# Optimization experiments

Hardware: AMD Instinct MI355X
Metric: run time of the kernel (lower is better)

The kernel has to match this reference:

```python
import jax, jax.numpy as jnp
import numpy as np

N_CLASSES = 5
N_SAMPLES = 512
D_EMB = 512


def setup_inputs() -> dict:
    key = jax.random.key(0)
    k1, k2, k3 = jax.random.split(key, 3)
    prediction = jax.random.normal(k1, (N_SAMPLES, D_EMB), dtype=jnp.float32)
    target = jax.random.randint(k2, (N_SAMPLES,), 0, N_CLASSES)
    # learnable_map=None -> all learnable, init = inverse_softplus(0.5 + 0.5*U[0,1))
    t = 0.5 + 0.5 * jax.random.uniform(k3, (N_CLASSES - 1,), dtype=jnp.float32)
    distances_raw = jnp.log(jnp.exp(t) - 1.0)  # inverse softplus (t < 20 always)
    return {"prediction": prediction, "distances_raw": distances_raw, "target": target}


def reference(prediction, distances_raw, target):
    n = prediction.shape[0]
    eps = 1e-8  # torch F.cosine_similarity eps
    xn = prediction / jnp.maximum(jnp.linalg.norm(prediction, axis=1, keepdims=True), eps)
    cos = xn @ xn.T  # [i, j] pairwise cosine similarity

    same = target[:, None] == target[None, :]          # label_diff <= 0
    positives = same & ~jnp.eye(n, dtype=bool)          # same label, not self
    negatives = ~same                                   # different label

    # ordinal class positions from softplus-parameterized gaps
    pos_d = jax.nn.softplus(distances_raw)
    class_pos = jnp.concatenate([jnp.zeros(1, dtype=pos_d.dtype), jnp.cumsum(pos_d)])
    cp = class_pos[target]
    margins = jnp.where(negatives, jnp.abs(cp[:, None] - cp[None, :]), 0.0)  # [i, j]

    # Original loop over anchor-positive columns k:
    #   n_pair_loss[k][i, j] = -cos[i, k] + cos[i, j] + margins[i, j]
    #   valid iff positives[i, k] and negatives[i, j]; invalid -> relu(-inf)=0
    base = cos + margins                                # [i, j]
    diff = base[:, None, :] - cos[:, :, None]           # [i, k, j]
    val = jnp.where(negatives[:, None, :], jax.nn.relu(diff), 0.0)
    s = jnp.where(positives, val.sum(axis=2), 0.0)      # [i, k]
    negcount = negatives.sum(axis=1)                    # [i]
    cnt = jnp.where(positives, negcount[:, None], 0)    # loss_mask2
    L = s / jnp.maximum(cnt, 1)                         # per (anchor i, positive k)

    # mean over nonzero entries (mean_n_pair_loss[mean_n_pair_loss != 0].mean())
    nz = (L != 0.0).sum()
    return L.sum() / jnp.maximum(nz, 1).astype(L.dtype)
```

## Files before the change

### kernel.cpp

```cpp
#include <hip/hip_runtime.h>
#include <math.h>

#define NS 512
#define DE 512
#define NCL 5
#define NBLK 256


__global__ __launch_bounds__(512, 2) void k_dots(const float* __restrict__ pred,
                                                 float* __restrict__ dotA,
                                                 float* __restrict__ dotB,
                                                 float* __restrict__ dg) {
    const int b = blockIdx.x;
    const int tid = threadIdx.x;
    const int iA = b, iB = b + 256;

    const int w = tid >> 6, lane = tid & 63;
    const int g = lane >> 4, s = lane & 15;

    const float4* pA = (const float4*)&pred[(size_t)iA * DE];
    const float4* pB = (const float4*)&pred[(size_t)iB * DE];
    float4 fA[8], fB[8];
#pragma unroll
    for (int p = 0; p < 8; p++) { fA[p] = pA[p * 16 + s]; fB[p] = pB[p * 16 + s]; }

#pragma unroll 4
    for (int t = 0; t < 16; t++) {
        const int j = w * 64 + t * 4 + g;
        const float4* rj = (const float4*)&pred[(size_t)j * DE];
        float4 x[8];
#pragma unroll
        for (int p = 0; p < 8; p++) x[p] = rj[p * 16 + s];
        float aA = 0.0f, aB = 0.0f, aS = 0.0f;
#pragma unroll
        for (int p = 0; p < 8; p++) {
            aA = fmaf(x[p].x, fA[p].x, aA); aA = fmaf(x[p].y, fA[p].y, aA);
            aA = fmaf(x[p].z, fA[p].z, aA); aA = fmaf(x[p].w, fA[p].w, aA);
            aB = fmaf(x[p].x, fB[p].x, aB); aB = fmaf(x[p].y, fB[p].y, aB);
            aB = fmaf(x[p].z, fB[p].z, aB); aB = fmaf(x[p].w, fB[p].w, aB);
            aS = fmaf(x[p].x, x[p].x, aS);  aS = fmaf(x[p].y, x[p].y, aS);
            aS = fmaf(x[p].z, x[p].z, aS);  aS = fmaf(x[p].w, x[p].w, aS);
        }
#pragma unroll
        for (int m = 1; m <= 8; m <<= 1) {
            aA += __shfl_xor(aA, m);
            aB += __shfl_xor(aB, m);
            aS += __shfl_xor(aS, m);
        }
        if (s == 0) {
            dotA[(size_t)b * NS + j] = aA;
            dotB[(size_t)b * NS + j] = aB;
            if (b == 0) dg[j] = aS;
        }
    }
}

__global__ __launch_bounds__(512) void k_loss(const float* __restrict__ dotA,
                                              const float* __restrict__ dotB,
                                              const float* __restrict__ dg,
                                              const int* __restrict__ target,
                                              const float* __restrict__ draw,
                                              unsigned int* __restrict__ ctrl,
                                              float* __restrict__ out) {
    const int b = blockIdx.x;
    const int tid = threadIdx.x;
    const int iA = b, iB = b + 256;

    __shared__ float  rn_s[NS];
    __shared__ float  ckA[NS], ckB[NS];
    __shared__ float4 v4sA[NS / 4], v4sB[NS / 4];
    __shared__ int    pkA[NS], pkB[NS];
    __shared__ float  spart[NS * 17];
    __shared__ float  redf[512];
    __shared__ int    redi[512];
    __shared__ unsigned int pcA, pcB;

    float* gsum = (float*)ctrl;
    unsigned int* gnz    = ctrl + 1;
    unsigned int* ticket = ctrl + 2;

    if (tid == 0) { pcA = 0u; pcB = 0u; }

    const int j = tid;
    const float da = dotA[(size_t)b * NS + j];
    const float db = dotB[(size_t)b * NS + j];
    const float ns = dg[j];
    const float rnj = 1.0f / fmaxf(sqrtf(ns), 1e-8f);
    rn_s[j] = rnj;

    float cp[NCL];
    cp[0] = 0.0f;
#pragma unroll
    for (int c = 0; c < NCL - 1; c++) cp[c + 1] = cp[c] + log1pf(expf(draw[c]));
    const int tiA = target[iA], tiB = target[iB];
    const float cpA = cp[tiA], cpB = cp[tiB];
    const int tj = target[j];
    const float cpj = cp[tj];
    __syncthreads();

    const float rniA = rn_s[iA], rniB = rn_s[iB];
    {
        float c0 = da * rniA * rnj;
        bool n0 = (tj != tiA);
        ckA[j] = c0;
        ((float*)v4sA)[j] = n0 ? (c0 + fabsf(cpA - cpj)) : -1e30f;
        if (!n0 && j != iA) pkA[atomicAdd(&pcA, 1u)] = j;
        redi[tid] = (n0 ? 1 : 0);
    }
    {
        float c0 = db * rniB * rnj;
        bool n0 = (tj != tiB);
        ckB[j] = c0;
        ((float*)v4sB)[j] = n0 ? (c0 + fabsf(cpB - cpj)) : -1e30f;
        if (!n0 && j != iB) pkB[atomicAdd(&pcB, 1u)] = j;
        redi[tid] += (n0 ? 1 : 0) << 16;
    }
    __syncthreads();
    for (int s2 = 256; s2 > 0; s2 >>= 1) {
        if (tid < s2) redi[tid] += redi[tid + s2];
        __syncthreads();
    }
    const int negA = redi[0] & 0xffff;
    const int negB = redi[0] >> 16;
    const unsigned int nposA = pcA, nposB = pcB;
    __syncthreads();

    const int kl = tid & 31, jc = tid >> 5;
    const float denA = (float)(negA > 1 ? negA : 1);
    const float denB = (float)(negB > 1 ? negB : 1);
    float contrib = 0.0f;
    int nzc = 0;

    {
        float4 vj[8];
#pragma unroll
        for (int t = 0; t < 8; t++) vj[t] = v4sA[jc * 8 + t];
        for (unsigned int p = kl; p < nposA; p += 32) {
            const float ckp = ckA[pkA[p]];
            float s0 = 0.0f, s1 = 0.0f;
#pragma unroll
            for (int t = 0; t < 8; t++) {
                float4 wv = vj[t];
                s0 += fmaxf(wv.x - ckp, 0.0f) + fmaxf(wv.y - ckp, 0.0f);
                s1 += fmaxf(wv.z - ckp, 0.0f) + fmaxf(wv.w - ckp, 0.0f);
            }
            spart[p * 17 + jc] = s0 + s1;
        }
        __syncthreads();
        for (unsigned int p = tid; p < nposA; p += 512) {
            float s0 = 0.0f;
#pragma unroll
            for (int q = 0; q < 16; q++) s0 += spart[p * 17 + q];
            contrib += s0 / denA;
            if (s0 != 0.0f) nzc++;
        }
        __syncthreads();
    }
    {
        float4 vj[8];
#pragma unroll
        for (int t = 0; t < 8; t++) vj[t] = v4sB[jc * 8 + t];
        for (unsigned int p = kl; p < nposB; p += 32) {
            const float ckp = ckB[pkB[p]];
            float s0 = 0.0f, s1 = 0.0f;
#pragma unroll
            for (int t = 0; t < 8; t++) {
                float4 wv = vj[t];
                s0 += fmaxf(wv.x - ckp, 0.0f) + fmaxf(wv.y - ckp, 0.0f);
                s1 += fmaxf(wv.z - ckp, 0.0f) + fmaxf(wv.w - ckp, 0.0f);
            }
            spart[p * 17 + jc] = s0 + s1;
        }
        __syncthreads();
        for (unsigned int p = tid; p < nposB; p += 512) {
            float s0 = 0.0f;
#pragma unroll
            for (int q = 0; q < 16; q++) s0 += spart[p * 17 + q];
            contrib += s0 / denB;
            if (s0 != 0.0f) nzc++;
        }
    }

    redf[tid] = contrib;
    redi[tid] = nzc;
    __syncthreads();
    for (int s2 = 256; s2 > 0; s2 >>= 1) {
        if (tid < s2) { redf[tid] += redf[tid + s2]; redi[tid] += redi[tid + s2]; }
        __syncthreads();
    }
    if (tid == 0) {
        if (redf[0] != 0.0f || redi[0] != 0) {
            atomicAdd(gsum, redf[0]);
            atomicAdd(gnz, (unsigned int)redi[0]);
        }
        __threadfence();
        unsigned int t = atomicAdd(ticket, 1u);
        if (t == (unsigned int)(NBLK - 1)) {
            float s0 = atomicAdd(gsum, 0.0f);
            unsigned int n = atomicAdd(gnz, 0u);
            out[0] = s0 / (float)(n > 1u ? n : 1u);
        }
    }
}

extern "C" void kernel_launch(void* const* d_in, const int* in_sizes, int n_in,
                              void* d_out, int out_size, void* d_ws, size_t ws_size,
                              hipStream_t stream) {
    const float* pred   = (const float*)d_in[0];
    const float* draw   = (const float*)d_in[1];
    const int*   target = (const int*)d_in[2];
    float* out = (float*)d_out;

    float* ws   = (float*)d_ws;
    float* dotA = ws;
    float* dotB = ws + NBLK * NS;
    float* dg   = ws + 2 * NBLK * NS;
    unsigned int* ctrl = (unsigned int*)(dg + NS);

    hipMemsetAsync(ctrl, 0, 4 * sizeof(unsigned int), stream);
    hipLaunchKernelGGL(k_dots, dim3(NBLK), dim3(512), 0, stream, pred, dotA, dotB, dg);
    hipLaunchKernelGGL(k_loss, dim3(NBLK), dim3(512), 0, stream,
                       dotA, dotB, dg, target, draw, ctrl, out);
}
```

Measured before the change: 87.73 us.

## Retile Gram kernel into 16x64 output tiles over a 2D grid

The dot-product kernel now computes a 16-row by 64-column block of the Gram matrix per workgroup on a 32x8 grid. Each thread holds two j-rows and 16 anchor rows in registers, so every loaded vector is reused across many outputs instead of recomputing two anchors against all 512 rows. Results are staged through shared memory for coalesced stores into a single dots matrix. This cuts redundant global loads, but the per-thread register footprint is much larger and there are many more cross-lane shuffle reductions.

```diff
diff --git a/kernel.cpp b/kernel.cpp
--- a/kernel.cpp
+++ b/kernel.cpp
@@ -8,55 +8,70 @@
 
 
 __global__ __launch_bounds__(512, 2) void k_dots(const float* __restrict__ pred,
-                                                 float* __restrict__ dotA,
-                                                 float* __restrict__ dotB,
+                                                 float* __restrict__ dots,
                                                  float* __restrict__ dg) {
-    const int b = blockIdx.x;
+    const int a0 = blockIdx.x * 16;
+    const int j0 = blockIdx.y * 64;
     const int tid = threadIdx.x;
-    const int iA = b, iB = b + 256;
-
     const int w = tid >> 6, lane = tid & 63;
     const int g = lane >> 4, s = lane & 15;
-
-    const float4* pA = (const float4*)&pred[(size_t)iA * DE];
-    const float4* pB = (const float4*)&pred[(size_t)iB * DE];
-    float4 fA[8], fB[8];
-#pragma unroll
-    for (int p = 0; p < 8; p++) { fA[p] = pA[p * 16 + s]; fB[p] = pB[p * 16 + s]; }
-
-#pragma unroll 4
-    for (int t = 0; t < 16; t++) {
-        const int j = w * 64 + t * 4 + g;
-        const float4* rj = (const float4*)&pred[(size_t)j * DE];
-        float4 x[8];
-#pragma unroll
-        for (int p = 0; p < 8; p++) x[p] = rj[p * 16 + s];
-        float aA = 0.0f, aB = 0.0f, aS = 0.0f;
-#pragma unroll
-        for (int p = 0; p < 8; p++) {
-            aA = fmaf(x[p].x, fA[p].x, aA); aA = fmaf(x[p].y, fA[p].y, aA);
-            aA = fmaf(x[p].z, fA[p].z, aA); aA = fmaf(x[p].w, fA[p].w, aA);
-            aB = fmaf(x[p].x, fB[p].x, aB); aB = fmaf(x[p].y, fB[p].y, aB);
-            aB = fmaf(x[p].z, fB[p].z, aB); aB = fmaf(x[p].w, fB[p].w, aB);
-            aS = fmaf(x[p].x, x[p].x, aS);  aS = fmaf(x[p].y, x[p].y, aS);
-            aS = fmaf(x[p].z, x[p].z, aS);  aS = fmaf(x[p].w, x[p].w, aS);
-        }
-#pragma unroll
-        for (int m = 1; m <= 8; m <<= 1) {
-            aA += __shfl_xor(aA, m);
-            aB += __shfl_xor(aB, m);
-            aS += __shfl_xor(aS, m);
-        }
-        if (s == 0) {
-            dotA[(size_t)b * NS + j] = aA;
-            dotB[(size_t)b * NS + j] = aB;
-            if (b == 0) dg[j] = aS;
-        }
-    }
+    const int jl0 = (w * 4 + g) * 2;
+
+    __shared__ float tile[16][65];
+    __shared__ float stile[64];
+
+    const float4* p4 = (const float4*)pred;
+    const float4* pj0 = p4 + (size_t)(j0 + jl0) * (DE / 4);
+    const float4* pj1 = p4 + (size_t)(j0 + jl0 + 1) * (DE / 4);
+
+    float acc0[17] = {};
+    float acc1[17] = {};
+
+#pragma unroll 2
+    for (int kb = 0; kb < 8; kb++) {
+        float4 fa[16];
+#pragma unroll
+        for (int a = 0; a < 16; a++)
+            fa[a] = p4[(size_t)(a0 + a) * (DE / 4) + kb * 16 + s];
+        float4 x0 = pj0[kb * 16 + s];
+        float4 x1 = pj1[kb * 16 + s];
+#pragma unroll
+        for (int a = 0; a < 16; a++) {
+            acc0[a] = fmaf(x0.x, fa[a].x, acc0[a]); acc0[a] = fmaf(x0.y, fa[a].y, acc0[a]);
+            acc0[a] = fmaf(x0.z, fa[a].z, acc0[a]); acc0[a] = fmaf(x0.w, fa[a].w, acc0[a]);
+            acc1[a] = fmaf(x1.x, fa[a].x, acc1[a]); acc1[a] = fmaf(x1.y, fa[a].y, acc1[a]);
+            acc1[a] = fmaf(x1.z, fa[a].z, acc1[a]); acc1[a] = fmaf(x1.w, fa[a].w, acc1[a]);
+        }
+        acc0[16] = fmaf(x0.x, x0.x, acc0[16]); acc0[16] = fmaf(x0.y, x0.y, acc0[16]);
+        acc0[16] = fmaf(x0.z, x0.z, acc0[16]); acc0[16] = fmaf(x0.w, x0.w, acc0[16]);
+        acc1[16] = fmaf(x1.x, x1.x, acc1[16]); acc1[16] = fmaf(x1.y, x1.y, acc1[16]);
+        acc1[16] = fmaf(x1.z, x1.z, acc1[16]); acc1[16] = fmaf(x1.w, x1.w, acc1[16]);
+    }
+
+#pragma unroll
+    for (int m = 1; m <= 8; m <<= 1) {
+#pragma unroll
+        for (int a = 0; a < 17; a++) {
+            acc0[a] += __shfl_xor(acc0[a], m);
+            acc1[a] += __shfl_xor(acc1[a], m);
+        }
+    }
+
+    tile[s][jl0]     = acc0[s];
+    tile[s][jl0 + 1] = acc1[s];
+    if (s == 0) { stile[jl0] = acc0[16]; stile[jl0 + 1] = acc1[16]; }
+    __syncthreads();
+
+#pragma unroll
+    for (int r = 0; r < 2; r++) {
+        int idx = tid + r * 512;
+        int a = idx >> 6, jl = idx & 63;
+        dots[(size_t)(a0 + a) * NS + j0 + jl] = tile[a][jl];
+    }
+    if (tid < 64) dg[j0 + tid] = stile[tid];
 }
 
-__global__ __launch_bounds__(512) void k_loss(const float* __restrict__ dotA,
-                                              const float* __restrict__ dotB,
+__global__ __launch_bounds__(512) void k_loss(const float* __restrict__ dots,
                                               const float* __restrict__ dg,
                                               const int* __restrict__ target,
                                               const float* __restrict__ draw,
@@ -82,8 +97,8 @@
     if (tid == 0) { pcA = 0u; pcB = 0u; }
 
     const int j = tid;
-    const float da = dotA[(size_t)b * NS + j];
-    const float db = dotB[(size_t)b * NS + j];
+    const float da = dots[(size_t)iA * NS + j];
+    const float db = dots[(size_t)iB * NS + j];
     const float ns = dg[j];
     const float rnj = 1.0f / fmaxf(sqrtf(ns), 1e-8f);
     rn_s[j] = rnj;
@@ -212,13 +227,12 @@
     float* out = (float*)d_out;
 
     float* ws   = (float*)d_ws;
-    float* dotA = ws;
-    float* dotB = ws + NBLK * NS;
-    float* dg   = ws + 2 * NBLK * NS;
+    float* dots = ws;
+    float* dg   = ws + NS * NS;
     unsigned int* ctrl = (unsigned int*)(dg + NS);
 
     hipMemsetAsync(ctrl, 0, 4 * sizeof(unsigned int), stream);
-    hipLaunchKernelGGL(k_dots, dim3(NBLK), dim3(512), 0, stream, pred, dotA, dotB, dg);
+    hipLaunchKernelGGL(k_dots, dim3(32, 8), dim3(512), 0, stream, pred, dots, dg);
     hipLaunchKernelGGL(k_loss, dim3(NBLK), dim3(512), 0, stream,
-                       dotA, dotB, dg, target, draw, ctrl, out);
+                       dots, dg, target, draw, ctrl, out);
 }
```

After: 90.24 us. +2.9%, slower.
